# Kernel optimization log

Hardware: AMD Instinct MI355X
Metric: run time of the kernel (lower is better)

Reference implementation:

```python
import jax, jax.numpy as jnp
import numpy as np

N_HEADS = 71
HEAD_DIM = 64
ROPE_BASE = 10000.0
SCALE = 1.0 / np.sqrt(HEAD_DIM)  # 0.125


def setup_inputs() -> dict:
    key = jax.random.key(0)
    k1, k2, k3 = jax.random.split(key, 3)
    B, S, H = 1, 1024, N_HEADS * HEAD_DIM  # 4544
    F = (N_HEADS + 2) * HEAD_DIM           # 4672 fused QKV out features
    hidden_states = jax.random.normal(k1, (B, 1, S, H), dtype=jnp.float32)
    qkv_weight = jax.random.normal(k2, (H, F), dtype=jnp.float32) * 0.02
    dense_weight = jax.random.normal(k3, (H, H), dtype=jnp.float32) * 0.02
    # additive causal mask [1,1,S,S]
    causal = np.tril(np.ones((S, S), dtype=bool))
    attention_mask = jnp.asarray(np.where(causal, 0.0, -1e9).astype(np.float32))[None, None]
    return {"hidden_states": hidden_states, "qkv_weight": qkv_weight,
            "dense_weight": dense_weight, "attention_mask": attention_mask}


def _rope_tables(seq_len):
    inv_freq = 1.0 / (ROPE_BASE ** (jnp.arange(0, HEAD_DIM, 2, dtype=jnp.float32) / HEAD_DIM))
    t = jnp.arange(seq_len, dtype=jnp.float32)
    freqs = t[:, None] * inv_freq[None, :]          # [S, 32]
    emb = jnp.concatenate([freqs, freqs], axis=-1)  # [S, 64]
    return jnp.cos(emb), jnp.sin(emb)


def _rotate_half(x):
    h = HEAD_DIM // 2
    return jnp.concatenate([-x[..., h:], x[..., :h]], axis=-1)


def reference(hidden_states, qkv_weight, dense_weight, attention_mask):
    # Prefill: hidden_states [B, 1, S, H]
    B, _, S, H = hidden_states.shape
    x = hidden_states[:, 0]                                  # [B, S, H]
    qkv = jnp.einsum('bsh,hf->bsf', x, qkv_weight)           # fused QKV matmul
    qd = N_HEADS * HEAD_DIM
    # Falcon-7B MQA head split: 71 query heads, 1 shared K and V head
    q = qkv[..., :qd].reshape(B, S, N_HEADS, HEAD_DIM).transpose(0, 2, 1, 3)  # [B, nH, S, d]
    k = qkv[..., qd:qd + HEAD_DIM]                           # [B, S, d]
    v = qkv[..., qd + HEAD_DIM:]                             # [B, S, d]
    cos, sin = _rope_tables(S)                               # [S, d]
    q = q * cos + _rotate_half(q) * sin
    k = k * cos + _rotate_half(k) * sin
    scores = jnp.einsum('bhqd,bkd->bhqk', q, k) * SCALE      # [B, nH, S, S]
    scores = scores + attention_mask                         # causal mask (alibi is None for Falcon-7B)
    probs = jax.nn.softmax(scores, axis=-1)
    ctx = jnp.einsum('bhqk,bkd->bhqd', probs, v)             # [B, nH, S, d]
    merged = ctx.transpose(0, 2, 1, 3).reshape(B, S, H)      # concat heads
    out = jnp.einsum('bsh,hf->bsf', merged, dense_weight)    # selfout dense
    return out[:, None]                                      # [B, 1, S, H]
```

## Files before the change

kernel.cpp:

```cpp
#include <hip/hip_runtime.h>
#include <hip/hip_bf16.h>

#define DI __device__ __forceinline__

typedef __attribute__((ext_vector_type(8))) short bf16x8;
typedef __attribute__((ext_vector_type(4))) float f32x4;
typedef __attribute__((ext_vector_type(4))) short s16x4;

constexpr int S  = 1024;
constexpr int NH = 71;
constexpr int HD = 64;
constexpr int H  = NH * HD;
constexpr int F  = (NH + 2) * HD;
constexpr float K2 = 0.125f * 1.44269504f;

DI short f2bf(float f) {
  union { float f; unsigned u; } v; v.f = f;
  unsigned r = v.u + 0x7fffu + ((v.u >> 16) & 1u);
  return (short)(r >> 16);
}
DI unsigned cvt_pk_bf16(float lo, float hi) {
  unsigned r;
  asm("v_cvt_pk_bf16_f32 %0, %1, %2" : "=v"(r) : "v"(lo), "v"(hi));
  return r;
}
DI float redmax_g(float x) {
  float y = fmaxf(x, __int_as_float(__builtin_amdgcn_ds_swizzle(__float_as_int(x), 0x401F)));
  return fmaxf(y, __shfl_xor(y, 32));
}
DI float redsum_g(float x) {
  float y = x + __int_as_float(__builtin_amdgcn_ds_swizzle(__float_as_int(x), 0x401F));
  return y + __shfl_xor(y, 32);
}

DI void gload_lds16(const void* g, void* l) {
  __builtin_amdgcn_global_load_lds(
      (const __attribute__((address_space(1))) unsigned int*)g,
      (__attribute__((address_space(3))) unsigned int*)l, 16, 0, 0);
}

DI bf16x8 ldswz(const char* base, int row, int slot) {
  return *(const bf16x8*)(base + row * 128 + ((slot ^ (row & 7)) << 4));
}

__global__ void cast_x_kernel(const float* __restrict__ x, short* __restrict__ xb, int n4) {
  int i = blockIdx.x * blockDim.x + threadIdx.x;
  if (i >= n4) return;
  f32x4 v = ((const f32x4*)x)[i];
  s16x4 o = { f2bf(v.x), f2bf(v.y), f2bf(v.z), f2bf(v.w) };
  ((s16x4*)xb)[i] = o;
}

__global__ __launch_bounds__(256) void transpose_cast_kernel(
    const float* __restrict__ W, short* __restrict__ Wt, int K, int N) {
  __shared__ float tile[64][65];
  int n0 = blockIdx.x * 64, k0 = blockIdx.y * 64;
  int c = threadIdx.x & 63, rg = threadIdx.x >> 6;
#pragma unroll
  for (int i = 0; i < 16; ++i) {
    int r = rg * 16 + i;
    tile[r][c] = W[(size_t)(k0 + r) * N + n0 + c];
  }
  __syncthreads();
#pragma unroll
  for (int i = 0; i < 16; ++i) {
    int r = rg * 16 + i;
    Wt[(size_t)(n0 + r) * K + k0 + c] = f2bf(tile[c][r]);
  }
}

__global__ void rope_tables_kernel(float* __restrict__ ct, float* __restrict__ st) {
  int s = blockIdx.x, i = threadIdx.x;
  float invf = powf(10000.0f, -(float)i / 32.0f);
  float a = (float)s * invf;
  ct[s * 32 + i] = cosf(a);
  st[s * 32 + i] = sinf(a);
}

__global__ __launch_bounds__(256) void rope_pack_kernel(
    const float* __restrict__ qkv, const float* __restrict__ ct, const float* __restrict__ st,
    short* __restrict__ Qb, short* __restrict__ Kb, short* __restrict__ Vt) {
  int s = blockIdx.x;
  const float* row = qkv + (size_t)s * F;
  for (int c = threadIdx.x; c < F; c += 256) {
    int hh = c >> 6, d = c & 63;
    float v = row[c];
    if (hh <= NH) {
      int i = d & 31;
      float cs = ct[s * 32 + i], sn = st[s * 32 + i];
      float rot = (d < 32) ? -row[c + 32] : row[c - 32];
      short ob = f2bf(v * cs + rot * sn);
      if (hh < NH) Qb[((size_t)hh * S + s) * 64 + d] = ob;
      else         Kb[(size_t)s * 64 + d] = ob;
    } else {
      Vt[(size_t)d * S + s] = f2bf(v);
    }
  }
}

__global__ __launch_bounds__(256, 3) void gemm_bt_kernel(
    const short* __restrict__ A, const short* __restrict__ Bt, float* __restrict__ C,
    int M, int N, int K) {
  __shared__ short As[2 * 128 * 64];
  __shared__ short Bs[2 * 64 * 64];
  const int tid = threadIdx.x;
  const int lane = tid & 63;
  const int wave = tid >> 6;
  const int wr = wave >> 1, wc = wave & 1;
  const int lr = lane & 15, g = lane >> 4;

  const int nwg = gridDim.x;
  int bid = blockIdx.x;
  int wgid = ((nwg & 7) == 0) ? ((bid & 7) * (nwg >> 3) + (bid >> 3)) : bid;
  const int ntm = M >> 7;
  const int tn = wgid / ntm;
  const int tm = wgid % ntm;

  f32x4 acc[4][2] = {};

  int srowA[4], skofA[4];
#pragma unroll
  for (int iss = 0; iss < 4; ++iss) {
    int d = iss * 256 + wave * 64 + lane;
    int row = (d >> 2) & 127;
    int c = (d & 3) ^ ((row >> 1) & 3);
    srowA[iss] = row;
    skofA[iss] = ((d >> 9) << 5) + c * 8;
  }
  int srowB[2], skofB[2];
#pragma unroll
  for (int iss = 0; iss < 2; ++iss) {
    int d = iss * 256 + wave * 64 + lane;
    int row = (d >> 2) & 63;
    int c = (d & 3) ^ ((row >> 1) & 3);
    srowB[iss] = row;
    skofB[iss] = ((d >> 8) << 5) + c * 8;
  }
  int offA[2][4], offB[2][2];
#pragma unroll
  for (int im = 0; im < 4; ++im) {
    int row_a = wr * 64 + im * 16 + lr;
    int sl = (g ^ ((row_a >> 1) & 3)) << 4;
#pragma unroll
    for (int kk = 0; kk < 2; ++kk) offA[kk][im] = kk * 8192 + row_a * 64 + sl;
  }
#pragma unroll
  for (int in = 0; in < 2; ++in) {
    int row_b = wc * 32 + in * 16 + lr;
    int sl = (g ^ ((row_b >> 1) & 3)) << 4;
#pragma unroll
    for (int kk = 0; kk < 2; ++kk) offB[kk][in] = kk * 4096 + row_b * 64 + sl;
  }

  char* AsB = (char*)As;
  char* BsB = (char*)Bs;
  const size_t Abase = (size_t)tm * 128 * K;
  const size_t Bbase = (size_t)tn * 64 * K;

#define STAGE(buf, k0)                                                                  \
  {                                                                                     \
    _Pragma("unroll")                                                                   \
    for (int iss = 0; iss < 4; ++iss)                                                   \
      gload_lds16(A + Abase + (size_t)srowA[iss] * K + (k0) + skofA[iss],               \
                  AsB + (buf) * 16384 + (iss * 4 + wave) * 1024);                       \
    _Pragma("unroll")                                                                   \
    for (int iss = 0; iss < 2; ++iss)                                                   \
      gload_lds16(Bt + Bbase + (size_t)srowB[iss] * K + (k0) + skofB[iss],              \
                  BsB + (buf) * 8192 + (iss * 4 + wave) * 1024);                        \
  }

  STAGE(0, 0);
  STAGE(1, 64);
  const int KS = K >> 6;
  for (int t = 0; t < KS; ++t) {
    const int cur = t & 1;
    if (t + 1 < KS) asm volatile("s_waitcnt vmcnt(6)" ::: "memory");
    else            asm volatile("s_waitcnt vmcnt(0)" ::: "memory");
    __builtin_amdgcn_sched_barrier(0);
    __builtin_amdgcn_s_barrier();
    __builtin_amdgcn_sched_barrier(0);
    const char* Ac = AsB + cur * 16384;
    const char* Bc = BsB + cur * 8192;
    bf16x8 af[2][4], bfr[2][2];
#pragma unroll
    for (int kk = 0; kk < 2; ++kk) {
#pragma unroll
      for (int im = 0; im < 4; ++im) af[kk][im] = *(const bf16x8*)(Ac + offA[kk][im]);
#pragma unroll
      for (int in = 0; in < 2; ++in) bfr[kk][in] = *(const bf16x8*)(Bc + offB[kk][in]);
    }
#pragma unroll
    for (int kk = 0; kk < 2; ++kk)
#pragma unroll
      for (int im = 0; im < 4; ++im)
#pragma unroll
        for (int in = 0; in < 2; ++in)
          acc[im][in] = __builtin_amdgcn_mfma_f32_16x16x32_bf16(af[kk][im], bfr[kk][in], acc[im][in], 0, 0, 0);
    __builtin_amdgcn_sched_barrier(0);
    __builtin_amdgcn_s_barrier();
    __builtin_amdgcn_sched_barrier(0);
    if (t + 2 < KS) STAGE(cur, (t + 2) << 6);
  }
#undef STAGE

#pragma unroll
  for (int im = 0; im < 4; ++im) {
#pragma unroll
    for (int in = 0; in < 2; ++in) {
      int row = tm * 128 + wr * 64 + im * 16 + g * 4;
      int col = tn * 64 + wc * 32 + in * 16 + lr;
#pragma unroll
      for (int i = 0; i < 4; ++i)
        C[(size_t)(row + i) * N + col] = acc[im][in][i];
    }
  }
}

DI void attn_step(const char* Kc, const char* Vc, char* P,
                  int key0, int qrow, bf16x8 aQ0, bf16x8 aQ1,
                  f32x4* accO, float& m, float& l, int lr, int g) {
  f32x4 p[4];
#pragma unroll
  for (int nf = 0; nf < 4; ++nf) {
    int row = nf * 16 + lr;
    bf16x8 k0 = ldswz(Kc, row, g);
    bf16x8 k1 = ldswz(Kc, row, g + 4);
    f32x4 z = {};
    z = __builtin_amdgcn_mfma_f32_16x16x32_bf16(k0, aQ0, z, 0, 0, 0);
    p[nf] = __builtin_amdgcn_mfma_f32_16x16x32_bf16(k1, aQ1, z, 0, 0, 0);
  }
  float pmx = -3e30f;
#pragma unroll
  for (int nf = 0; nf < 4; ++nf)
#pragma unroll
    for (int i = 0; i < 4; ++i) {
      int key = key0 + nf * 16 + 4 * g + i;
      float sv = p[nf][i] * K2 + (key <= qrow ? 0.0f : -1e30f);
      p[nf][i] = sv;
      pmx = fmaxf(pmx, sv);
    }
  float pm = redmax_g(pmx);
  float mn = fmaxf(m, pm);
  float scl = __builtin_exp2f(m - mn);
  m = mn;
  float rsx = 0.f;
#pragma unroll
  for (int nf = 0; nf < 4; ++nf) {
    f32x4 pe;
#pragma unroll
    for (int i = 0; i < 4; ++i) {
      pe[i] = __builtin_exp2f(p[nf][i] - m);
      rsx += pe[i];
    }
    uint2 wv;
    wv.x = cvt_pk_bf16(pe[0], pe[1]);
    wv.y = cvt_pk_bf16(pe[2], pe[3]);
    *(uint2*)(P + lr * 144 + nf * 32 + g * 8) = wv;
  }
  float rs = redsum_g(rsx);
  l = l * scl + rs;
#pragma unroll
  for (int df = 0; df < 4; ++df)
#pragma unroll
    for (int i = 0; i < 4; ++i)
      accO[df][i] *= scl;
#pragma unroll
  for (int st = 0; st < 2; ++st) {
    bf16x8 bP = *(const bf16x8*)(P + lr * 144 + st * 64 + g * 16);
#pragma unroll
    for (int df = 0; df < 4; ++df) {
      bf16x8 aV = ldswz(Vc, df * 16 + lr, g + 4 * st);
      accO[df] = __builtin_amdgcn_mfma_f32_16x16x32_bf16(aV, bP, accO[df], 0, 0, 0);
    }
  }
}

__global__ __launch_bounds__(256) void attn_kernel(
    const short* __restrict__ Qb,
    const short* __restrict__ Kb,
    const short* __restrict__ Vt,
    short* __restrict__ merged) {
  __shared__ short Ks[2][4096];
  __shared__ short Vs[2][4096];
  __shared__ short Ps[4][16 * 72];
  const int lane = threadIdx.x & 63, w = threadIdx.x >> 6;
  const int lr = lane & 15, g = lane >> 4;
  const int j = blockIdx.x, head = blockIdx.y;
  const int kbmax = 15 - j;
  const int qA = j * 64 + w * 16 + lr;
  const int qB = (15 - j) * 64 + w * 16 + lr;
  char* KsB = (char*)Ks;
  char* VsB = (char*)Vs;
  char* P = (char*)Ps[w];

  int crow[2], cslot[2];
#pragma unroll
  for (int i = 0; i < 2; ++i) {
    int c = (i * 4 + w) * 64 + lane;
    crow[i] = c >> 3;
    cslot[i] = (c & 7) ^ (crow[i] & 7);
  }

  const short* qap = Qb + ((size_t)head * S + qA) * 64 + g * 8;
  bf16x8 aQA0 = *(const bf16x8*)(qap);
  bf16x8 aQA1 = *(const bf16x8*)(qap + 32);
  const short* qbp = Qb + ((size_t)head * S + qB) * 64 + g * 8;
  bf16x8 aQB0 = *(const bf16x8*)(qbp);
  bf16x8 aQB1 = *(const bf16x8*)(qbp + 32);

  f32x4 accA[4] = {}, accB[4] = {};
  float mA = -3e30f, lA = 0.f, mB = -3e30f, lB = 0.f;

#define STAGEKV(buf, key0)                                                       \
  {                                                                              \
    _Pragma("unroll")                                                            \
    for (int i = 0; i < 2; ++i) {                                                \
      gload_lds16(Kb + (size_t)((key0) + crow[i]) * 64 + cslot[i] * 8,           \
                  KsB + (buf) * 8192 + (i * 4 + w) * 1024);                      \
      gload_lds16(Vt + (size_t)crow[i] * S + (key0) + cslot[i] * 8,              \
                  VsB + (buf) * 8192 + (i * 4 + w) * 1024);                      \
    }                                                                            \
  }

  STAGEKV(0, 0);
  for (int kb = 0; kb <= kbmax; ++kb) {
    const int cur = kb & 1;
    __syncthreads();
    if (kb < kbmax) STAGEKV(cur ^ 1, (kb + 1) * 64);
    const char* Kc = KsB + cur * 8192;
    const char* Vc = VsB + cur * 8192;
    attn_step(Kc, Vc, P, kb * 64, qB, aQB0, aQB1, accB, mB, lB, lr, g);
    if (kb <= j)
      attn_step(Kc, Vc, P, kb * 64, qA, aQA0, aQA1, accA, mA, lA, lr, g);
  }
#undef STAGEKV

  float rlA = 1.0f / lA, rlB = 1.0f / lB;
#pragma unroll
  for (int df = 0; df < 4; ++df)
#pragma unroll
    for (int i = 0; i < 4; ++i) {
      int d = head * 64 + df * 16 + 4 * g + i;
      merged[(size_t)qB * H + d] = f2bf(accB[df][i] * rlB);
      merged[(size_t)qA * H + d] = f2bf(accA[df][i] * rlA);
    }
}

extern "C" void kernel_launch(void* const* d_in, const int* in_sizes, int n_in,
                              void* d_out, int out_size, void* d_ws, size_t ws_size,
                              hipStream_t stream) {
  const float* x    = (const float*)d_in[0];
  const float* wqkv = (const float*)d_in[1];
  const float* wd   = (const float*)d_in[2];
  float* out = (float*)d_out;

  char* ws = (char*)d_ws;
  size_t off = 0;
  short* Wqkvt  = (short*)(ws + off); off += (size_t)F * H * 2;
  short* Wdt    = (short*)(ws + off); off += (size_t)H * H * 2;
  short* Qb     = (short*)(ws + off); off += (size_t)NH * S * HD * 2;
  short* Kb     = (short*)(ws + off); off += (size_t)S * HD * 2;
  short* Vtb    = (short*)(ws + off); off += (size_t)HD * S * 2;
  short* merged = (short*)(ws + off); off += (size_t)S * H * 2;
  float* ct     = (float*)(ws + off); off += (size_t)S * 32 * 4;
  float* st     = (float*)(ws + off); off += (size_t)S * 32 * 4;
  short* xb     = (short*)(ws + off); off += (size_t)S * H * 2;
  float* qkv    = (float*)(ws + off); off += (size_t)S * F * 4;
  (void)ws_size; (void)in_sizes; (void)n_in; (void)out_size;

  hipLaunchKernelGGL(cast_x_kernel, dim3((S * H / 4 + 255) / 256), dim3(256), 0, stream,
                     x, xb, S * H / 4);
  hipLaunchKernelGGL(transpose_cast_kernel, dim3(F / 64, H / 64), dim3(256), 0, stream,
                     wqkv, Wqkvt, H, F);
  hipLaunchKernelGGL(transpose_cast_kernel, dim3(H / 64, H / 64), dim3(256), 0, stream,
                     wd, Wdt, H, H);
  hipLaunchKernelGGL(rope_tables_kernel, dim3(S), dim3(32), 0, stream, ct, st);
  hipLaunchKernelGGL(gemm_bt_kernel, dim3((F / 64) * (S / 128)), dim3(256), 0, stream,
                     xb, Wqkvt, qkv, S, F, H);
  hipLaunchKernelGGL(rope_pack_kernel, dim3(S), dim3(256), 0, stream,
                     qkv, ct, st, Qb, Kb, Vtb);
  hipLaunchKernelGGL(attn_kernel, dim3(8, NH), dim3(256), 0, stream,
                     Qb, Kb, Vtb, merged);
  hipLaunchKernelGGL(gemm_bt_kernel, dim3((H / 64) * (S / 128)), dim3(256), 0, stream,
                     merged, Wdt, out, S, H, H);
}
```

Baseline: 244.1 us.

## Triple-buffer GEMM loads, merge weight transposes, fold RoPE tables into pack

```diff
diff --git a/kernel.cpp b/kernel.cpp
--- a/kernel.cpp
+++ b/kernel.cpp
@@ -51,10 +51,21 @@
   ((s16x4*)xb)[i] = o;
 }
 
-__global__ __launch_bounds__(256) void transpose_cast_kernel(
-    const float* __restrict__ W, short* __restrict__ Wt, int K, int N) {
+__global__ __launch_bounds__(256) void transpose2_kernel(
+    const float* __restrict__ W1, short* __restrict__ Wt1,
+    const float* __restrict__ W2, short* __restrict__ Wt2) {
   __shared__ float tile[64][65];
-  int n0 = blockIdx.x * 64, k0 = blockIdx.y * 64;
+  const int nb1 = (F / 64) * (H / 64);
+  int bid = blockIdx.x;
+  const float* W; short* Wt; int N, n0, k0;
+  if (bid < nb1) {
+    W = W1; Wt = Wt1; N = F;
+    n0 = (bid % (F / 64)) * 64; k0 = (bid / (F / 64)) * 64;
+  } else {
+    bid -= nb1;
+    W = W2; Wt = Wt2; N = H;
+    n0 = (bid % (H / 64)) * 64; k0 = (bid / (H / 64)) * 64;
+  }
   int c = threadIdx.x & 63, rg = threadIdx.x >> 6;
 #pragma unroll
   for (int i = 0; i < 16; ++i) {
@@ -65,31 +76,30 @@
 #pragma unroll
   for (int i = 0; i < 16; ++i) {
     int r = rg * 16 + i;
-    Wt[(size_t)(n0 + r) * K + k0 + c] = f2bf(tile[c][r]);
-  }
-}
-
-__global__ void rope_tables_kernel(float* __restrict__ ct, float* __restrict__ st) {
-  int s = blockIdx.x, i = threadIdx.x;
-  float invf = powf(10000.0f, -(float)i / 32.0f);
-  float a = (float)s * invf;
-  ct[s * 32 + i] = cosf(a);
-  st[s * 32 + i] = sinf(a);
+    Wt[(size_t)(n0 + r) * H + k0 + c] = f2bf(tile[c][r]);
+  }
 }
 
 __global__ __launch_bounds__(256) void rope_pack_kernel(
-    const float* __restrict__ qkv, const float* __restrict__ ct, const float* __restrict__ st,
+    const float* __restrict__ qkv,
     short* __restrict__ Qb, short* __restrict__ Kb, short* __restrict__ Vt) {
+  __shared__ float cs[32], sn[32];
   int s = blockIdx.x;
+  if (threadIdx.x < 32) {
+    float invf = powf(10000.0f, -(float)threadIdx.x / 32.0f);
+    float a = (float)s * invf;
+    cs[threadIdx.x] = cosf(a);
+    sn[threadIdx.x] = sinf(a);
+  }
+  __syncthreads();
   const float* row = qkv + (size_t)s * F;
   for (int c = threadIdx.x; c < F; c += 256) {
     int hh = c >> 6, d = c & 63;
     float v = row[c];
     if (hh <= NH) {
       int i = d & 31;
-      float cs = ct[s * 32 + i], sn = st[s * 32 + i];
       float rot = (d < 32) ? -row[c + 32] : row[c - 32];
-      short ob = f2bf(v * cs + rot * sn);
+      short ob = f2bf(v * cs[i] + rot * sn[i]);
       if (hh < NH) Qb[((size_t)hh * S + s) * 64 + d] = ob;
       else         Kb[(size_t)s * 64 + d] = ob;
     } else {
@@ -98,11 +108,11 @@
   }
 }
 
-__global__ __launch_bounds__(256, 3) void gemm_bt_kernel(
+__global__ __launch_bounds__(256, 2) void gemm_bt_kernel(
     const short* __restrict__ A, const short* __restrict__ Bt, float* __restrict__ C,
     int M, int N, int K) {
-  __shared__ short As[2 * 128 * 64];
-  __shared__ short Bs[2 * 64 * 64];
+  __shared__ short As[3 * 128 * 64];
+  __shared__ short Bs[3 * 64 * 64];
   const int tid = threadIdx.x;
   const int lane = tid & 63;
   const int wave = tid >> 6;
@@ -157,25 +167,27 @@
   const size_t Abase = (size_t)tm * 128 * K;
   const size_t Bbase = (size_t)tn * 64 * K;
 
-#define STAGE(buf, k0)                                                                  \
+#define STAGE(buf, t)                                                                   \
   {                                                                                     \
     _Pragma("unroll")                                                                   \
     for (int iss = 0; iss < 4; ++iss)                                                   \
-      gload_lds16(A + Abase + (size_t)srowA[iss] * K + (k0) + skofA[iss],               \
+      gload_lds16(A + Abase + (size_t)srowA[iss] * K + ((t) << 6) + skofA[iss],         \
                   AsB + (buf) * 16384 + (iss * 4 + wave) * 1024);                       \
     _Pragma("unroll")                                                                   \
     for (int iss = 0; iss < 2; ++iss)                                                   \
-      gload_lds16(Bt + Bbase + (size_t)srowB[iss] * K + (k0) + skofB[iss],              \
+      gload_lds16(Bt + Bbase + (size_t)srowB[iss] * K + ((t) << 6) + skofB[iss],        \
                   BsB + (buf) * 8192 + (iss * 4 + wave) * 1024);                        \
   }
 
   STAGE(0, 0);
-  STAGE(1, 64);
+  STAGE(1, 1);
+  STAGE(2, 2);
   const int KS = K >> 6;
+  int cur = 0;
   for (int t = 0; t < KS; ++t) {
-    const int cur = t & 1;
-    if (t + 1 < KS) asm volatile("s_waitcnt vmcnt(6)" ::: "memory");
-    else            asm volatile("s_waitcnt vmcnt(0)" ::: "memory");
+    if (t + 2 < KS)      asm volatile("s_waitcnt vmcnt(12)" ::: "memory");
+    else if (t + 1 < KS) asm volatile("s_waitcnt vmcnt(6)" ::: "memory");
+    else                 asm volatile("s_waitcnt vmcnt(0)" ::: "memory");
     __builtin_amdgcn_sched_barrier(0);
     __builtin_amdgcn_s_barrier();
     __builtin_amdgcn_sched_barrier(0);
@@ -189,6 +201,7 @@
 #pragma unroll
       for (int in = 0; in < 2; ++in) bfr[kk][in] = *(const bf16x8*)(Bc + offB[kk][in]);
     }
+    __builtin_amdgcn_s_setprio(1);
 #pragma unroll
     for (int kk = 0; kk < 2; ++kk)
 #pragma unroll
@@ -196,10 +209,12 @@
 #pragma unroll
         for (int in = 0; in < 2; ++in)
           acc[im][in] = __builtin_amdgcn_mfma_f32_16x16x32_bf16(af[kk][im], bfr[kk][in], acc[im][in], 0, 0, 0);
+    __builtin_amdgcn_s_setprio(0);
     __builtin_amdgcn_sched_barrier(0);
     __builtin_amdgcn_s_barrier();
     __builtin_amdgcn_sched_barrier(0);
-    if (t + 2 < KS) STAGE(cur, (t + 2) << 6);
+    if (t + 3 < KS) STAGE(cur, t + 3);
+    cur = (cur == 2) ? 0 : cur + 1;
   }
 #undef STAGE
 
@@ -362,23 +377,19 @@
   short* Kb     = (short*)(ws + off); off += (size_t)S * HD * 2;
   short* Vtb    = (short*)(ws + off); off += (size_t)HD * S * 2;
   short* merged = (short*)(ws + off); off += (size_t)S * H * 2;
-  float* ct     = (float*)(ws + off); off += (size_t)S * 32 * 4;
-  float* st     = (float*)(ws + off); off += (size_t)S * 32 * 4;
   short* xb     = (short*)(ws + off); off += (size_t)S * H * 2;
   float* qkv    = (float*)(ws + off); off += (size_t)S * F * 4;
   (void)ws_size; (void)in_sizes; (void)n_in; (void)out_size;
 
   hipLaunchKernelGGL(cast_x_kernel, dim3((S * H / 4 + 255) / 256), dim3(256), 0, stream,
                      x, xb, S * H / 4);
-  hipLaunchKernelGGL(transpose_cast_kernel, dim3(F / 64, H / 64), dim3(256), 0, stream,
-                     wqkv, Wqkvt, H, F);
-  hipLaunchKernelGGL(transpose_cast_kernel, dim3(H / 64, H / 64), dim3(256), 0, stream,
-                     wd, Wdt, H, H);
-  hipLaunchKernelGGL(rope_tables_kernel, dim3(S), dim3(32), 0, stream, ct, st);
+  hipLaunchKernelGGL(transpose2_kernel,
+                     dim3((F / 64) * (H / 64) + (H / 64) * (H / 64)), dim3(256), 0, stream,
+                     wqkv, Wqkvt, wd, Wdt);
   hipLaunchKernelGGL(gemm_bt_kernel, dim3((F / 64) * (S / 128)), dim3(256), 0, stream,
                      xb, Wqkvt, qkv, S, F, H);
   hipLaunchKernelGGL(rope_pack_kernel, dim3(S), dim3(256), 0, stream,
-                     qkv, ct, st, Qb, Kb, Vtb);
+                     qkv, Qb, Kb, Vtb);
   hipLaunchKernelGGL(attn_kernel, dim3(8, NH), dim3(256), 0, stream,
                      Qb, Kb, Vtb, merged);
   hipLaunchKernelGGL(gemm_bt_kernel, dim3((H / 64) * (S / 128)), dim3(256), 0, stream,
```

Measured after the change: 328.0 us. 1.34x slower.
